# Performance work log

Hardware: AMD Instinct MI355X
Metric: run time of the kernel (lower is better)

## Reference

```python
import jax, jax.numpy as jnp
import numpy as np

N_NODES = 100000
N_EDGES = 1600000
D_FEAT = 64
D_OUT = 64


def setup_inputs() -> dict:
    key = jax.random.key(0)
    k1, k2, k3, k4 = jax.random.split(key, 4)
    vertices = jax.random.normal(k1, (N_NODES, D_FEAT), dtype=jnp.float32)
    edges = jax.random.randint(k2, (2, N_EDGES), 0, N_NODES, dtype=jnp.int64)
    weight = jax.random.normal(k3, (D_OUT, D_FEAT), dtype=jnp.float32) * (1.0 / np.sqrt(D_FEAT))
    bias = jax.random.normal(k4, (D_OUT,), dtype=jnp.float32) * 0.01
    return {"vertices": vertices, "edges": edges, "weight": weight, "bias": bias}


def reference(vertices, edges, weight, bias):
    # GraphConv forward, dense (non-sparse) path, self_loop=True, normalize=True.
    n_vertices = vertices.shape[0]
    idx = jnp.arange(n_vertices, dtype=edges.dtype)
    dst = jnp.concatenate([edges[0], idx])  # scatter destinations (edges[0])
    src = jnp.concatenate([edges[1], idx])  # gather sources (edges[1])
    # agg[i] = sum over edges with dst==i of vertices[src]
    agg = jax.ops.segment_sum(vertices[src], dst, num_segments=n_vertices)
    # degree per node (torch scatters ones_like(neighbours): all feature cols equal)
    deg = jax.ops.segment_sum(
        jnp.ones_like(dst, dtype=vertices.dtype), dst, num_segments=n_vertices
    )
    agg = agg * (jnp.clip(deg, 1.0, None) ** -0.5)[:, None]
    # Linear: y = agg @ W.T + b
    return agg @ weight.T + bias
```

## Files before the change

### kernel.cpp

```cpp
#include <hip/hip_runtime.h>
#include <hip/hip_fp16.h>

constexpr int N_NODES = 100000;
constexpr int N_EDGES = 1600000;
constexpr int D = 64;

constexpr int SH2    = 7;
constexpr int BSZ    = 1 << SH2;
constexpr int NB     = (N_NODES + BSZ - 1) / BSZ;
constexpr int SPLITB = 256;
constexpr int TILE   = (N_EDGES + SPLITB - 1) / SPLITB;
constexpr int LINB   = 2048;

constexpr int SCAN_CHUNK = 1024;
constexpr int NCHUNK = (N_NODES + SCAN_CHUNK - 1) / SCAN_CHUNK;

__global__ __launch_bounds__(256) void lin_hist(
    const float* __restrict__ vertices,
    const float* __restrict__ weight,
    __half* __restrict__ Yh,
    const int* __restrict__ edges,
    int* __restrict__ H)
{
    if (blockIdx.x < LINB) {
        __shared__ float rowbuf[4][64];
        const int wid  = threadIdx.x >> 6;
        const int lane = threadIdx.x & 63;

        float w[64];
        #pragma unroll
        for (int f = 0; f < 64; ++f) w[f] = weight[lane * 64 + f];

        const int nodesPerIter = LINB * 4;
        for (int base = blockIdx.x * 4; base < N_NODES; base += nodesPerIter) {
            const int node = base + wid;
            float a = 0.0f;
            if (node < N_NODES) a = vertices[(size_t)node * D + lane];
            rowbuf[wid][lane] = a;
            __syncthreads();
            float acc = 0.0f;
            #pragma unroll
            for (int f = 0; f < 64; ++f)
                acc += rowbuf[wid][f] * w[f];
            if (node < N_NODES) Yh[(size_t)node * D + lane] = __float2half(acc);
            __syncthreads();
        }
    } else {
        __shared__ int h[NB];
        const int b = blockIdx.x - LINB;
        for (int i = threadIdx.x; i < NB; i += 256) h[i] = 0;
        __syncthreads();
        const int lo = b * TILE;
        const int hi = min(lo + TILE, N_EDGES);
        for (int e = lo + threadIdx.x; e < hi; e += 256)
            atomicAdd(&h[edges[e] >> SH2], 1);
        __syncthreads();
        for (int i = threadIdx.x; i < NB; i += 256)
            H[b * NB + i] = h[i];
    }
}

__global__ __launch_bounds__(256) void s_scanA(int* __restrict__ H,
                                               int* __restrict__ colsum)
{
    const int j = blockIdx.x;
    const int t = threadIdx.x;
    int v = H[t * NB + j];
    __shared__ int s[256];
    s[t] = v; __syncthreads();
    for (int o = 1; o < 256; o <<= 1) {
        int u = (t >= o) ? s[t - o] : 0;
        __syncthreads();
        s[t] += u;
        __syncthreads();
    }
    H[t * NB + j] = s[t] - v;
    if (t == 255) colsum[j] = s[t];
}

__global__ void s_scanB(const int* __restrict__ colsum, int* __restrict__ bbase)
{
    __shared__ int s[256];
    const int t = threadIdx.x;
    int v[4]; int loc = 0;
    #pragma unroll
    for (int k = 0; k < 4; ++k) {
        int i = t * 4 + k;
        v[k] = (i < NB) ? colsum[i] : 0;
        loc += v[k];
    }
    s[t] = loc; __syncthreads();
    for (int o = 1; o < 256; o <<= 1) {
        int u = (t >= o) ? s[t - o] : 0;
        __syncthreads();
        s[t] += u;
        __syncthreads();
    }
    int excl = s[t] - loc;
    #pragma unroll
    for (int k = 0; k < 4; ++k) {
        int i = t * 4 + k;
        if (i < NB) bbase[i] = excl;
        excl += v[k];
    }
}

__global__ __launch_bounds__(256) void s_scatter(const int* __restrict__ edges,
                                                 const int* __restrict__ H,
                                                 const int* __restrict__ bbase,
                                                 int* __restrict__ packed)
{
    __shared__ int cur[NB];
    for (int i = threadIdx.x; i < NB; i += 256)
        cur[i] = bbase[i] + H[blockIdx.x * NB + i];
    __syncthreads();
    const int lo = blockIdx.x * TILE;
    const int hi = min(lo + TILE, N_EDGES);
    for (int e = lo + threadIdx.x; e < hi; e += 256) {
        int dst = edges[e];
        int src = edges[N_EDGES + e];
        int pos = atomicAdd(&cur[dst >> SH2], 1);
        packed[pos] = (src << SH2) | (dst & (BSZ - 1));
    }
}

__global__ __launch_bounds__(256) void bucket_csr(const int* __restrict__ packed,
                                                  const int* __restrict__ bbase,
                                                  const int* __restrict__ colsum,
                                                  int* __restrict__ offsets,
                                                  int* __restrict__ deg,
                                                  int* __restrict__ srt)
{
    __shared__ int h2[BSZ];
    __shared__ int cur2[BSZ];
    __shared__ int s[BSZ];
    const int b = blockIdx.x;
    const int t = threadIdx.x;
    const int start = bbase[b];
    const int cnt   = colsum[b];

    if (t < BSZ) h2[t] = 0;
    __syncthreads();
    for (int i = t; i < cnt; i += 256)
        atomicAdd(&h2[packed[start + i] & (BSZ - 1)], 1);
    __syncthreads();

    if (t < BSZ) s[t] = h2[t];
    __syncthreads();
    for (int o = 1; o < BSZ; o <<= 1) {
        int u = (t >= o && t < BSZ) ? s[t - o] : 0;
        __syncthreads();
        if (t < BSZ) s[t] += u;
        __syncthreads();
    }
    if (t < BSZ) {
        int excl = s[t] - h2[t];
        int node = (b << SH2) + t;
        if (node < N_NODES) { offsets[node] = start + excl; deg[node] = h2[t]; }
        cur2[t] = excl;
    }
    __syncthreads();

    for (int i = t; i < cnt; i += 256) {
        int p = packed[start + i];
        int r = atomicAdd(&cur2[p & (BSZ - 1)], 1);
        srt[start + r] = p >> SH2;
    }
}

__device__ __forceinline__ void addrow(float* acc, uint4 u)
{
    const __half2* h = reinterpret_cast<const __half2*>(&u);
    #pragma unroll
    for (int k = 0; k < 4; ++k) {
        float2 f = __half22float2(h[k]);
        acc[2 * k]     += f.x;
        acc[2 * k + 1] += f.y;
    }
}

__global__ __launch_bounds__(256) void gather_h(
    const __half* __restrict__ Yh,
    const int* __restrict__ offsets,
    const int* __restrict__ deg,
    const int* __restrict__ srt,
    const float* __restrict__ bias,
    float* __restrict__ out)
{
    const int wid  = threadIdx.x >> 6;
    const int lane = threadIdx.x & 63;
    const int g    = lane >> 3;
    const int sub  = lane & 7;
    const int node = blockIdx.x * 4 + wid;
    if (node >= N_NODES) return;

    const int start = offsets[node];
    const int cnt   = deg[node];

    float acc[8];
    #pragma unroll
    for (int j = 0; j < 8; ++j) acc[j] = 0.0f;

    if (g == 0) {
        uint4 u = *reinterpret_cast<const uint4*>(Yh + (size_t)node * D + sub * 8);
        addrow(acc, u);
    }

    int e = 0;
    for (; e + 16 <= cnt; e += 16) {
        int s0 = srt[start + e + g];
        int s1 = srt[start + e + 8 + g];
        uint4 u0 = *reinterpret_cast<const uint4*>(Yh + (size_t)s0 * D + sub * 8);
        uint4 u1 = *reinterpret_cast<const uint4*>(Yh + (size_t)s1 * D + sub * 8);
        addrow(acc, u0);
        addrow(acc, u1);
    }
    if (e + 8 <= cnt) {
        int s0 = srt[start + e + g];
        uint4 u0 = *reinterpret_cast<const uint4*>(Yh + (size_t)s0 * D + sub * 8);
        addrow(acc, u0);
        e += 8;
    }
    if (e + g < cnt) {
        int s0 = srt[start + e + g];
        uint4 u0 = *reinterpret_cast<const uint4*>(Yh + (size_t)s0 * D + sub * 8);
        addrow(acc, u0);
    }

    #pragma unroll
    for (int j = 0; j < 8; ++j) {
        acc[j] += __shfl_xor(acc[j], 8, 64);
        acc[j] += __shfl_xor(acc[j], 16, 64);
        acc[j] += __shfl_xor(acc[j], 32, 64);
    }

    if (g == 0) {
        const float sc = rsqrtf((float)cnt + 1.0f);
        const float4 b0 = *reinterpret_cast<const float4*>(bias + sub * 8);
        const float4 b1 = *reinterpret_cast<const float4*>(bias + sub * 8 + 4);
        float4 r0, r1;
        r0.x = acc[0] * sc + b0.x;  r0.y = acc[1] * sc + b0.y;
        r0.z = acc[2] * sc + b0.z;  r0.w = acc[3] * sc + b0.w;
        r1.x = acc[4] * sc + b1.x;  r1.y = acc[5] * sc + b1.y;
        r1.z = acc[6] * sc + b1.z;  r1.w = acc[7] * sc + b1.w;
        *reinterpret_cast<float4*>(out + (size_t)node * D + sub * 8)     = r0;
        *reinterpret_cast<float4*>(out + (size_t)node * D + sub * 8 + 4) = r1;
    }
}


__global__ __launch_bounds__(256) void linear_kernel(
    const float* __restrict__ vertices,
    const float* __restrict__ weight,
    float* __restrict__ Y)
{
    __shared__ float rowbuf[4][64];
    const int wid  = threadIdx.x >> 6;
    const int lane = threadIdx.x & 63;
    float w[64];
    #pragma unroll
    for (int f = 0; f < 64; ++f) w[f] = weight[lane * 64 + f];
    const int nodesPerIter = gridDim.x * 4;
    for (int base = blockIdx.x * 4; base < N_NODES; base += nodesPerIter) {
        const int node = base + wid;
        float a = 0.0f;
        if (node < N_NODES) a = vertices[(size_t)node * D + lane];
        rowbuf[wid][lane] = a;
        __syncthreads();
        float acc = 0.0f;
        #pragma unroll
        for (int f = 0; f < 64; ++f)
            acc += rowbuf[wid][f] * w[f];
        if (node < N_NODES) Y[(size_t)node * D + lane] = acc;
        __syncthreads();
    }
}

__global__ __launch_bounds__(256) void gather_f32(
    const float* __restrict__ Y,
    const int* __restrict__ offsets,
    const int* __restrict__ deg,
    const int* __restrict__ sortedSrc,
    const float* __restrict__ bias,
    float* __restrict__ out)
{
    const int wid  = threadIdx.x >> 6;
    const int lane = threadIdx.x & 63;
    const int g    = lane >> 4;
    const int sub  = lane & 15;
    const int node = blockIdx.x * 4 + wid;
    if (node >= N_NODES) return;

    const int start = offsets[node];
    const int cnt   = deg[node];

    float4 acc;
    if (g == 0) {
        acc = *reinterpret_cast<const float4*>(Y + (size_t)node * D + (sub << 2));
    } else {
        acc.x = 0.0f; acc.y = 0.0f; acc.z = 0.0f; acc.w = 0.0f;
    }

    int e = 0;
    for (; e + 8 <= cnt; e += 8) {
        int s0 = sortedSrc[start + e + g];
        int s1 = sortedSrc[start + e + 4 + g];
        const float4 a0 = *reinterpret_cast<const float4*>(Y + (size_t)s0 * D + (sub << 2));
        const float4 a1 = *reinterpret_cast<const float4*>(Y + (size_t)s1 * D + (sub << 2));
        acc.x += a0.x; acc.y += a0.y; acc.z += a0.z; acc.w += a0.w;
        acc.x += a1.x; acc.y += a1.y; acc.z += a1.z; acc.w += a1.w;
    }
    if (e + 4 <= cnt) {
        int s0 = sortedSrc[start + e + g];
        const float4 a0 = *reinterpret_cast<const float4*>(Y + (size_t)s0 * D + (sub << 2));
        acc.x += a0.x; acc.y += a0.y; acc.z += a0.z; acc.w += a0.w;
        e += 4;
    }
    if (e + g < cnt) {
        int s0 = sortedSrc[start + e + g];
        const float4 a0 = *reinterpret_cast<const float4*>(Y + (size_t)s0 * D + (sub << 2));
        acc.x += a0.x; acc.y += a0.y; acc.z += a0.z; acc.w += a0.w;
    }

    acc.x += __shfl_xor(acc.x, 16, 64);
    acc.y += __shfl_xor(acc.y, 16, 64);
    acc.z += __shfl_xor(acc.z, 16, 64);
    acc.w += __shfl_xor(acc.w, 16, 64);
    acc.x += __shfl_xor(acc.x, 32, 64);
    acc.y += __shfl_xor(acc.y, 32, 64);
    acc.z += __shfl_xor(acc.z, 32, 64);
    acc.w += __shfl_xor(acc.w, 32, 64);

    if (lane < 16) {
        const float sc = rsqrtf((float)cnt + 1.0f);
        const float4 b4 = *reinterpret_cast<const float4*>(bias + (sub << 2));
        float4 r;
        r.x = acc.x * sc + b4.x;
        r.y = acc.y * sc + b4.y;
        r.z = acc.z * sc + b4.z;
        r.w = acc.w * sc + b4.w;
        *reinterpret_cast<float4*>(out + (size_t)node * D + (sub << 2)) = r;
    }
}

__global__ __launch_bounds__(256) void hist_kernel(const int* __restrict__ edges,
                                                   int* __restrict__ deg)
{
    int e = blockIdx.x * 256 + threadIdx.x;
    if (e < N_EDGES) atomicAdd(&deg[edges[e]], 1);
}

__global__ __launch_bounds__(256) void scan_part(const int* __restrict__ deg,
                                                 int* __restrict__ partial)
{
    int t = threadIdx.x;
    int base = blockIdx.x * SCAN_CHUNK + t * 4;
    int s = 0;
    #pragma unroll
    for (int k = 0; k < 4; ++k) { int i = base + k; if (i < N_NODES) s += deg[i]; }
    int lane = t & 63, wid = t >> 6;
    #pragma unroll
    for (int off = 32; off; off >>= 1) s += __shfl_down(s, off, 64);
    __shared__ int red[4];
    if (lane == 0) red[wid] = s;
    __syncthreads();
    if (t == 0) partial[blockIdx.x] = red[0] + red[1] + red[2] + red[3];
}

__device__ __forceinline__ int waveInclScan(int v, int lane) {
    #pragma unroll
    for (int off = 1; off < 64; off <<= 1) {
        int t = __shfl_up(v, off, 64);
        if (lane >= off) v += t;
    }
    return v;
}

__global__ void scan_small(int* partial) {
    int lane = threadIdx.x;
    int v0 = (lane < NCHUNK) ? partial[lane] : 0;
    int v1 = (64 + lane < NCHUNK) ? partial[64 + lane] : 0;
    int i0 = waveInclScan(v0, lane);
    int tot0 = __shfl(i0, 63, 64);
    int i1 = waveInclScan(v1, lane) + tot0;
    if (lane < NCHUNK) partial[lane] = i0 - v0;
    if (64 + lane < NCHUNK) partial[64 + lane] = i1 - v1;
}

__global__ __launch_bounds__(256) void scan_final(const int* __restrict__ deg,
                                                  const int* __restrict__ partial,
                                                  int* __restrict__ offsets,
                                                  int* __restrict__ cursor)
{
    int t = threadIdx.x;
    int base = blockIdx.x * SCAN_CHUNK + t * 4;
    int d[4]; int s = 0;
    #pragma unroll
    for (int k = 0; k < 4; ++k) { int i = base + k; d[k] = (i < N_NODES) ? deg[i] : 0; s += d[k]; }
    __shared__ int sd[256];
    sd[t] = s; __syncthreads();
    #pragma unroll
    for (int off = 1; off < 256; off <<= 1) {
        int v = (t >= off) ? sd[t - off] : 0;
        __syncthreads();
        sd[t] += v;
        __syncthreads();
    }
    int excl = sd[t] - s + partial[blockIdx.x];
    #pragma unroll
    for (int k = 0; k < 4; ++k) {
        int i = base + k;
        if (i < N_NODES) { offsets[i] = excl; cursor[i] = excl; excl += d[k]; }
    }
}

__global__ __launch_bounds__(256) void scatter_idx(const int* __restrict__ edges,
                                                   int* __restrict__ cursor,
                                                   int* __restrict__ sortedSrc)
{
    int e = blockIdx.x * 256 + threadIdx.x;
    if (e >= N_EDGES) return;
    int dst = edges[e];
    int src = edges[N_EDGES + e];
    int pos = atomicAdd(&cursor[dst], 1);
    sortedSrc[pos] = src;
}


__global__ __launch_bounds__(256) void fb_scatter(
    const float* __restrict__ vertices, const int* __restrict__ edges,
    float* __restrict__ agg, float* __restrict__ degF)
{
    long long tid = (long long)blockIdx.x * 256 + threadIdx.x;
    int lane = threadIdx.x & 63;
    long long e = tid >> 6;
    if (e >= N_EDGES) return;
    int dst = edges[e];
    int src = edges[N_EDGES + e];
    atomicAdd(&agg[(size_t)dst * D + lane], vertices[(size_t)src * D + lane]);
    if (lane == 0) atomicAdd(&degF[dst], 1.0f);
}

__global__ __launch_bounds__(256) void fb_finish(
    const float* __restrict__ vertices, const float* __restrict__ weight,
    const float* __restrict__ bias, const float* __restrict__ degF,
    float* __restrict__ out)
{
    __shared__ float rowbuf[4][64];
    const int wid  = threadIdx.x >> 6;
    const int lane = threadIdx.x & 63;
    float w[64];
    #pragma unroll
    for (int f = 0; f < 64; ++f) w[f] = weight[lane * 64 + f];
    const float b = bias[lane];
    const int nodesPerIter = gridDim.x * 4;
    for (int base = blockIdx.x * 4; base < N_NODES; base += nodesPerIter) {
        const int node = base + wid;
        float a = 0.0f;
        if (node < N_NODES) {
            const float scale = rsqrtf(degF[node] + 1.0f);
            a = (out[(size_t)node * D + lane] + vertices[(size_t)node * D + lane]) * scale;
        }
        rowbuf[wid][lane] = a;
        __syncthreads();
        float acc = b;
        #pragma unroll
        for (int f = 0; f < 64; ++f) acc += rowbuf[wid][f] * w[f];
        if (node < N_NODES) out[(size_t)node * D + lane] = acc;
        __syncthreads();
    }
}

extern "C" void kernel_launch(void* const* d_in, const int* in_sizes, int n_in,
                              void* d_out, int out_size, void* d_ws, size_t ws_size,
                              hipStream_t stream) {
    const float* vertices = (const float*)d_in[0];
    const int*   edges    = (const int*)d_in[1];
    const float* weight   = (const float*)d_in[2];
    const float* bias     = (const float*)d_in[3];
    float* out = (float*)d_out;

    const int threads = 256;
    const int edgeBlocks = (N_EDGES + threads - 1) / threads;

    {
        __half* Yh    = (__half*)d_ws;
        int*   H      = (int*)(Yh + (size_t)N_NODES * D);
        int*   colsum = H + SPLITB * NB;
        int*   bbase  = colsum + NB;
        int*   offs   = bbase + NB;
        int*   deg    = offs + N_NODES;
        int*   packed = deg + N_NODES;
        int*   srt    = packed + N_EDGES;
        size_t needed = (size_t)((char*)(srt + N_EDGES) - (char*)d_ws);
        if (ws_size >= needed) {
            lin_hist<<<LINB + SPLITB, threads, 0, stream>>>(vertices, weight, Yh, edges, H);
            s_scanA<<<NB, threads, 0, stream>>>(H, colsum);
            s_scanB<<<1, threads, 0, stream>>>(colsum, bbase);
            s_scatter<<<SPLITB, threads, 0, stream>>>(edges, H, bbase, packed);
            bucket_csr<<<NB, threads, 0, stream>>>(packed, bbase, colsum, offs, deg, srt);
            gather_h<<<(N_NODES + 3) / 4, threads, 0, stream>>>(Yh, offs, deg, srt, bias, out);
            return;
        }
    }

    {
        float* Y       = (float*)d_ws;
        int*   deg     = (int*)(Y + (size_t)N_NODES * D);
        int*   offs    = deg + N_NODES;
        int*   cursor  = offs + N_NODES;
        int*   partial = cursor + N_NODES;
        int*   srt     = partial + 128;
        size_t needed  = (size_t)((char*)(srt + N_EDGES) - (char*)d_ws);
        if (ws_size >= needed) {
            hipMemsetAsync(deg, 0, sizeof(int) * N_NODES, stream);
            linear_kernel<<<1024, threads, 0, stream>>>(vertices, weight, Y);
            hist_kernel<<<edgeBlocks, threads, 0, stream>>>(edges, deg);
            scan_part<<<NCHUNK, threads, 0, stream>>>(deg, partial);
            scan_small<<<1, 64, 0, stream>>>(partial);
            scan_final<<<NCHUNK, threads, 0, stream>>>(deg, partial, offs, cursor);
            scatter_idx<<<edgeBlocks, threads, 0, stream>>>(edges, cursor, srt);
            gather_f32<<<(N_NODES + 3) / 4, threads, 0, stream>>>(Y, offs, deg, srt, bias, out);
            return;
        }
    }

    {
        float* degF = (float*)d_ws;
        hipMemsetAsync(out, 0, sizeof(float) * (size_t)N_NODES * D, stream);
        hipMemsetAsync(degF, 0, sizeof(float) * N_NODES, stream);
        const long long totalScatter = (long long)N_EDGES * 64;
        fb_scatter<<<(int)((totalScatter + threads - 1) / threads), threads, 0, stream>>>(
            vertices, edges, out, degF);
        fb_finish<<<1024, threads, 0, stream>>>(vertices, weight, bias, degF, out);
    }
}
```

Measured before the change: 116.2 us.

## Fuse bucket CSR build with gather and fold bucket scan into scatter

Shrinks buckets to 64 nodes and fuses the per-bucket counting sort with the neighbor gather, so sorted source indices stay in shared memory (with a global fallback when a bucket exceeds capacity) rather than being written and re-read through offsets/deg/srt arrays. The separate bucket-base scan kernel is removed; every scatter block redundantly scans the column sums itself, and block 0 writes bbase. The linear/histogram kernel moves to 1024-thread blocks with float4 shared reads. This saves two launches and global round-trips, but adds redundant scan work in each scatter block and puts both the per-bucket sort and the gather inside one block with serialized phases.

```diff
diff --git a/kernel.cpp b/kernel.cpp
--- a/kernel.cpp
+++ b/kernel.cpp
@@ -5,17 +5,18 @@
 constexpr int N_EDGES = 1600000;
 constexpr int D = 64;
 
-constexpr int SH2    = 7;
+constexpr int SH2    = 6;
 constexpr int BSZ    = 1 << SH2;
 constexpr int NB     = (N_NODES + BSZ - 1) / BSZ;
 constexpr int SPLITB = 256;
 constexpr int TILE   = (N_EDGES + SPLITB - 1) / SPLITB;
-constexpr int LINB   = 2048;
+constexpr int LINB   = 512;
+constexpr int SRTCAP = 2048;
 
 constexpr int SCAN_CHUNK = 1024;
 constexpr int NCHUNK = (N_NODES + SCAN_CHUNK - 1) / SCAN_CHUNK;
 
-__global__ __launch_bounds__(256) void lin_hist(
+__global__ __launch_bounds__(1024) void lin_hist(
     const float* __restrict__ vertices,
     const float* __restrict__ weight,
     __half* __restrict__ Yh,
@@ -23,7 +24,7 @@
     int* __restrict__ H)
 {
     if (blockIdx.x < LINB) {
-        __shared__ float rowbuf[4][64];
+        __shared__ float rowbuf[16][64];
         const int wid  = threadIdx.x >> 6;
         const int lane = threadIdx.x & 63;
 
@@ -31,31 +32,34 @@
         #pragma unroll
         for (int f = 0; f < 64; ++f) w[f] = weight[lane * 64 + f];
 
-        const int nodesPerIter = LINB * 4;
-        for (int base = blockIdx.x * 4; base < N_NODES; base += nodesPerIter) {
+        const int nodesPerIter = LINB * 16;
+        for (int base = blockIdx.x * 16; base < N_NODES; base += nodesPerIter) {
             const int node = base + wid;
             float a = 0.0f;
             if (node < N_NODES) a = vertices[(size_t)node * D + lane];
             rowbuf[wid][lane] = a;
             __syncthreads();
             float acc = 0.0f;
+            const float4* rb4 = reinterpret_cast<const float4*>(&rowbuf[wid][0]);
             #pragma unroll
-            for (int f = 0; f < 64; ++f)
-                acc += rowbuf[wid][f] * w[f];
+            for (int f4 = 0; f4 < 16; ++f4) {
+                float4 r = rb4[f4];
+                acc += r.x * w[4*f4] + r.y * w[4*f4+1] + r.z * w[4*f4+2] + r.w * w[4*f4+3];
+            }
             if (node < N_NODES) Yh[(size_t)node * D + lane] = __float2half(acc);
             __syncthreads();
         }
     } else {
         __shared__ int h[NB];
         const int b = blockIdx.x - LINB;
-        for (int i = threadIdx.x; i < NB; i += 256) h[i] = 0;
+        for (int i = threadIdx.x; i < NB; i += 1024) h[i] = 0;
         __syncthreads();
         const int lo = b * TILE;
         const int hi = min(lo + TILE, N_EDGES);
-        for (int e = lo + threadIdx.x; e < hi; e += 256)
+        for (int e = lo + threadIdx.x; e < hi; e += 1024)
             atomicAdd(&h[edges[e] >> SH2], 1);
         __syncthreads();
-        for (int i = threadIdx.x; i < NB; i += 256)
+        for (int i = threadIdx.x; i < NB; i += 1024)
             H[b * NB + i] = h[i];
     }
 }
@@ -78,45 +82,40 @@
     if (t == 255) colsum[j] = s[t];
 }
 
-__global__ void s_scanB(const int* __restrict__ colsum, int* __restrict__ bbase)
-{
-    __shared__ int s[256];
+__global__ __launch_bounds__(1024) void s_scatter(const int* __restrict__ edges,
+                                                  const int* __restrict__ H,
+                                                  const int* __restrict__ colsum,
+                                                  int* __restrict__ packed,
+                                                  int* __restrict__ bbase)
+{
+    __shared__ int cur[NB];
+    __shared__ int sd[1024];
     const int t = threadIdx.x;
-    int v[4]; int loc = 0;
-    #pragma unroll
-    for (int k = 0; k < 4; ++k) {
-        int i = t * 4 + k;
-        v[k] = (i < NB) ? colsum[i] : 0;
-        loc += v[k];
-    }
-    s[t] = loc; __syncthreads();
-    for (int o = 1; o < 256; o <<= 1) {
-        int u = (t >= o) ? s[t - o] : 0;
-        __syncthreads();
-        s[t] += u;
-        __syncthreads();
-    }
-    int excl = s[t] - loc;
-    #pragma unroll
-    for (int k = 0; k < 4; ++k) {
-        int i = t * 4 + k;
-        if (i < NB) bbase[i] = excl;
-        excl += v[k];
-    }
-}
-
-__global__ __launch_bounds__(256) void s_scatter(const int* __restrict__ edges,
-                                                 const int* __restrict__ H,
-                                                 const int* __restrict__ bbase,
-                                                 int* __restrict__ packed)
-{
-    __shared__ int cur[NB];
-    for (int i = threadIdx.x; i < NB; i += 256)
-        cur[i] = bbase[i] + H[blockIdx.x * NB + i];
+
+    int v0 = (2*t     < NB) ? colsum[2*t]     : 0;
+    int v1 = (2*t + 1 < NB) ? colsum[2*t + 1] : 0;
+    int pair = v0 + v1;
+    sd[t] = pair; __syncthreads();
+    for (int o = 1; o < 1024; o <<= 1) {
+        int u = (t >= o) ? sd[t - o] : 0;
+        __syncthreads();
+        sd[t] += u;
+        __syncthreads();
+    }
+    int excl = sd[t] - pair;
+    if (2*t < NB) {
+        cur[2*t] = excl + H[blockIdx.x * NB + 2*t];
+        if (blockIdx.x == 0) bbase[2*t] = excl;
+    }
+    if (2*t + 1 < NB) {
+        cur[2*t + 1] = excl + v0 + H[blockIdx.x * NB + 2*t + 1];
+        if (blockIdx.x == 0) bbase[2*t + 1] = excl + v0;
+    }
     __syncthreads();
+
     const int lo = blockIdx.x * TILE;
     const int hi = min(lo + TILE, N_EDGES);
-    for (int e = lo + threadIdx.x; e < hi; e += 256) {
+    for (int e = lo + t; e < hi; e += 1024) {
         int dst = edges[e];
         int src = edges[N_EDGES + e];
         int pos = atomicAdd(&cur[dst >> SH2], 1);
@@ -124,50 +123,6 @@
     }
 }
 
-__global__ __launch_bounds__(256) void bucket_csr(const int* __restrict__ packed,
-                                                  const int* __restrict__ bbase,
-                                                  const int* __restrict__ colsum,
-                                                  int* __restrict__ offsets,
-                                                  int* __restrict__ deg,
-                                                  int* __restrict__ srt)
-{
-    __shared__ int h2[BSZ];
-    __shared__ int cur2[BSZ];
-    __shared__ int s[BSZ];
-    const int b = blockIdx.x;
-    const int t = threadIdx.x;
-    const int start = bbase[b];
-    const int cnt   = colsum[b];
-
-    if (t < BSZ) h2[t] = 0;
-    __syncthreads();
-    for (int i = t; i < cnt; i += 256)
-        atomicAdd(&h2[packed[start + i] & (BSZ - 1)], 1);
-    __syncthreads();
-
-    if (t < BSZ) s[t] = h2[t];
-    __syncthreads();
-    for (int o = 1; o < BSZ; o <<= 1) {
-        int u = (t >= o && t < BSZ) ? s[t - o] : 0;
-        __syncthreads();
-        if (t < BSZ) s[t] += u;
-        __syncthreads();
-    }
-    if (t < BSZ) {
-        int excl = s[t] - h2[t];
-        int node = (b << SH2) + t;
-        if (node < N_NODES) { offsets[node] = start + excl; deg[node] = h2[t]; }
-        cur2[t] = excl;
-    }
-    __syncthreads();
-
-    for (int i = t; i < cnt; i += 256) {
-        int p = packed[start + i];
-        int r = atomicAdd(&cur2[p & (BSZ - 1)], 1);
-        srt[start + r] = p >> SH2;
-    }
-}
-
 __device__ __forceinline__ void addrow(float* acc, uint4 u)
 {
     const __half2* h = reinterpret_cast<const __half2*>(&u);
@@ -179,72 +134,148 @@
     }
 }
 
-__global__ __launch_bounds__(256) void gather_h(
+__device__ __forceinline__ int waveInclScan(int v, int lane) {
+    #pragma unroll
+    for (int off = 1; off < 64; off <<= 1) {
+        int t = __shfl_up(v, off, 64);
+        if (lane >= off) v += t;
+    }
+    return v;
+}
+
+__global__ __launch_bounds__(256) void csr_gather(
+    const int* __restrict__ packed,
+    const int* __restrict__ bbase,
+    const int* __restrict__ colsum,
     const __half* __restrict__ Yh,
-    const int* __restrict__ offsets,
-    const int* __restrict__ deg,
-    const int* __restrict__ srt,
     const float* __restrict__ bias,
+    int* __restrict__ srtG,
     float* __restrict__ out)
 {
-    const int wid  = threadIdx.x >> 6;
-    const int lane = threadIdx.x & 63;
+    __shared__ int h[BSZ];
+    __shared__ int excl[BSZ];
+    __shared__ int cur[BSZ];
+    __shared__ int srtL[SRTCAP];
+
+    const int t = threadIdx.x;
+    const int b = blockIdx.x;
+    const int start = bbase[b];
+    const int cnt   = colsum[b];
+
+    if (t < BSZ) h[t] = 0;
+    __syncthreads();
+    for (int i = t; i < cnt; i += 256)
+        atomicAdd(&h[packed[start + i] & (BSZ - 1)], 1);
+    __syncthreads();
+    if (t < BSZ) {
+        int v = h[t];
+        int incl = waveInclScan(v, t);
+        excl[t] = incl - v;
+        cur[t]  = incl - v;
+    }
+    __syncthreads();
+    const bool useG = (cnt > SRTCAP);
+    if (!useG) {
+        for (int i = t; i < cnt; i += 256) {
+            int p = packed[start + i];
+            int r = atomicAdd(&cur[p & (BSZ - 1)], 1);
+            srtL[r] = p >> SH2;
+        }
+    } else {
+        for (int i = t; i < cnt; i += 256) {
+            int p = packed[start + i];
+            int r = atomicAdd(&cur[p & (BSZ - 1)], 1);
+            srtG[start + r] = p >> SH2;
+        }
+    }
+    __syncthreads();
+
+    const int wid  = t >> 6;
+    const int lane = t & 63;
     const int g    = lane >> 3;
     const int sub  = lane & 7;
-    const int node = blockIdx.x * 4 + wid;
-    if (node >= N_NODES) return;
-
-    const int start = offsets[node];
-    const int cnt   = deg[node];
-
-    float acc[8];
-    #pragma unroll
-    for (int j = 0; j < 8; ++j) acc[j] = 0.0f;
-
-    if (g == 0) {
-        uint4 u = *reinterpret_cast<const uint4*>(Yh + (size_t)node * D + sub * 8);
-        addrow(acc, u);
-    }
-
-    int e = 0;
-    for (; e + 16 <= cnt; e += 16) {
-        int s0 = srt[start + e + g];
-        int s1 = srt[start + e + 8 + g];
-        uint4 u0 = *reinterpret_cast<const uint4*>(Yh + (size_t)s0 * D + sub * 8);
-        uint4 u1 = *reinterpret_cast<const uint4*>(Yh + (size_t)s1 * D + sub * 8);
-        addrow(acc, u0);
-        addrow(acc, u1);
-    }
-    if (e + 8 <= cnt) {
-        int s0 = srt[start + e + g];
-        uint4 u0 = *reinterpret_cast<const uint4*>(Yh + (size_t)s0 * D + sub * 8);
-        addrow(acc, u0);
-        e += 8;
-    }
-    if (e + g < cnt) {
-        int s0 = srt[start + e + g];
-        uint4 u0 = *reinterpret_cast<const uint4*>(Yh + (size_t)s0 * D + sub * 8);
-        addrow(acc, u0);
-    }
-
-    #pragma unroll
-    for (int j = 0; j < 8; ++j) {
-        acc[j] += __shfl_xor(acc[j], 8, 64);
-        acc[j] += __shfl_xor(acc[j], 16, 64);
-        acc[j] += __shfl_xor(acc[j], 32, 64);
-    }
-
-    if (g == 0) {
-        const float sc = rsqrtf((float)cnt + 1.0f);
-        const float4 b0 = *reinterpret_cast<const float4*>(bias + sub * 8);
-        const float4 b1 = *reinterpret_cast<const float4*>(bias + sub * 8 + 4);
-        float4 r0, r1;
-        r0.x = acc[0] * sc + b0.x;  r0.y = acc[1] * sc + b0.y;
-        r0.z = acc[2] * sc + b0.z;  r0.w = acc[3] * sc + b0.w;
-        r1.x = acc[4] * sc + b1.x;  r1.y = acc[5] * sc + b1.y;
-        r1.z = acc[6] * sc + b1.z;  r1.w = acc[7] * sc + b1.w;
-        *reinterpret_cast<float4*>(out + (size_t)node * D + sub * 8)     = r0;
-        *reinterpret_cast<float4*>(out + (size_t)node * D + sub * 8 + 4) = r1;
+
+    const float4 b0 = *reinterpret_cast<const float4*>(bias + sub * 8);
+    const float4 b1 = *reinterpret_cast<const float4*>(bias + sub * 8 + 4);
+
+    for (int m = 0; m < 16; ++m) {
+        const int l = wid * 16 + m;
+        const int node = (b << SH2) + l;
+        if (node >= N_NODES) break;
+
+        const int off = excl[l];
+        const int dc  = h[l];
+
+        float acc[8];
+        #pragma unroll
+        for (int j = 0; j < 8; ++j) acc[j] = 0.0f;
+
+        if (g == 0) {
+            uint4 u = *reinterpret_cast<const uint4*>(Yh + (size_t)node * D + sub * 8);
+            addrow(acc, u);
+        }
+
+        int e = 0;
+        if (!useG) {
+            for (; e + 16 <= dc; e += 16) {
+                int s0 = srtL[off + e + g];
+                int s1 = srtL[off + e + 8 + g];
+                uint4 u0 = *reinterpret_cast<const uint4*>(Yh + (size_t)s0 * D + sub * 8);
+                uint4 u1 = *reinterpret_cast<const uint4*>(Yh + (size_t)s1 * D + sub * 8);
+                addrow(acc, u0);
+                addrow(acc, u1);
+            }
+            if (e + 8 <= dc) {
+                int s0 = srtL[off + e + g];
+                uint4 u0 = *reinterpret_cast<const uint4*>(Yh + (size_t)s0 * D + sub * 8);
+                addrow(acc, u0);
+                e += 8;
+            }
+            if (e + g < dc) {
+                int s0 = srtL[off + e + g];
+                uint4 u0 = *reinterpret_cast<const uint4*>(Yh + (size_t)s0 * D + sub * 8);
+                addrow(acc, u0);
+            }
+        } else {
+            const int* srt = srtG + start;
+            for (; e + 16 <= dc; e += 16) {
+                int s0 = srt[off + e + g];
+                int s1 = srt[off + e + 8 + g];
+                uint4 u0 = *reinterpret_cast<const uint4*>(Yh + (size_t)s0 * D + sub * 8);
+                uint4 u1 = *reinterpret_cast<const uint4*>(Yh + (size_t)s1 * D + sub * 8);
+                addrow(acc, u0);
+                addrow(acc, u1);
+            }
+            if (e + 8 <= dc) {
+                int s0 = srt[off + e + g];
+                uint4 u0 = *reinterpret_cast<const uint4*>(Yh + (size_t)s0 * D + sub * 8);
+                addrow(acc, u0);
+                e += 8;
+            }
+            if (e + g < dc) {
+                int s0 = srt[off + e + g];
+                uint4 u0 = *reinterpret_cast<const uint4*>(Yh + (size_t)s0 * D + sub * 8);
+                addrow(acc, u0);
+            }
+        }
+
+        #pragma unroll
+        for (int j = 0; j < 8; ++j) {
+            acc[j] += __shfl_xor(acc[j], 8, 64);
+            acc[j] += __shfl_xor(acc[j], 16, 64);
+            acc[j] += __shfl_xor(acc[j], 32, 64);
+        }
+
+        if (g == 0) {
+            const float sc = rsqrtf((float)dc + 1.0f);
+            float4 r0, r1;
+            r0.x = acc[0] * sc + b0.x;  r0.y = acc[1] * sc + b0.y;
+            r0.z = acc[2] * sc + b0.z;  r0.w = acc[3] * sc + b0.w;
+            r1.x = acc[4] * sc + b1.x;  r1.y = acc[5] * sc + b1.y;
+            r1.z = acc[6] * sc + b1.z;  r1.w = acc[7] * sc + b1.w;
+            *reinterpret_cast<float4*>(out + (size_t)node * D + sub * 8)     = r0;
+            *reinterpret_cast<float4*>(out + (size_t)node * D + sub * 8 + 4) = r1;
+        }
     }
 }
 
@@ -367,15 +398,6 @@
     if (t == 0) partial[blockIdx.x] = red[0] + red[1] + red[2] + red[3];
 }
 
-__device__ __forceinline__ int waveInclScan(int v, int lane) {
-    #pragma unroll
-    for (int off = 1; off < 64; off <<= 1) {
-        int t = __shfl_up(v, off, 64);
-        if (lane >= off) v += t;
-    }
-    return v;
-}
-
 __global__ void scan_small(int* partial) {
     int lane = threadIdx.x;
     int v0 = (lane < NCHUNK) ? partial[lane] : 0;
@@ -488,18 +510,14 @@
         int*   H      = (int*)(Yh + (size_t)N_NODES * D);
         int*   colsum = H + SPLITB * NB;
         int*   bbase  = colsum + NB;
-        int*   offs   = bbase + NB;
-        int*   deg    = offs + N_NODES;
-        int*   packed = deg + N_NODES;
-        int*   srt    = packed + N_EDGES;
-        size_t needed = (size_t)((char*)(srt + N_EDGES) - (char*)d_ws);
+        int*   packed = bbase + NB;
+        int*   srtG   = packed + N_EDGES;
+        size_t needed = (size_t)((char*)(srtG + N_EDGES) - (char*)d_ws);
         if (ws_size >= needed) {
-            lin_hist<<<LINB + SPLITB, threads, 0, stream>>>(vertices, weight, Yh, edges, H);
+            lin_hist<<<LINB + SPLITB, 1024, 0, stream>>>(vertices, weight, Yh, edges, H);
             s_scanA<<<NB, threads, 0, stream>>>(H, colsum);
-            s_scanB<<<1, threads, 0, stream>>>(colsum, bbase);
-            s_scatter<<<SPLITB, threads, 0, stream>>>(edges, H, bbase, packed);
-            bucket_csr<<<NB, threads, 0, stream>>>(packed, bbase, colsum, offs, deg, srt);
-            gather_h<<<(N_NODES + 3) / 4, threads, 0, stream>>>(Yh, offs, deg, srt, bias, out);
+            s_scatter<<<SPLITB, 1024, 0, stream>>>(edges, H, colsum, packed, bbase);
+            csr_gather<<<NB, threads, 0, stream>>>(packed, bbase, colsum, Yh, bias, srtG, out);
             return;
         }
     }
```

After: 141.3 us. 21.6% more time.

## Replace per-block histogram scan with global atomic bucket counts and tile cursors

Applied to the files above, without the earlier changes.

The two-level counting sort no longer stores a per-block histogram matrix and scans it column-wise. Blocks now add their local bucket counts into a global count array with atomics, a single 512-thread kernel scans the counts, and the scatter kernel reserves a range per tile through atomics on a global cursor. Bucket size drops from 128 to 64 nodes, so the in-bucket scan becomes a wave shuffle scan. This removes two kernels and the large histogram traffic, at the cost of a memset, more global atomics, and a nondeterministic edge order within each bucket.

```diff
diff --git a/kernel.cpp b/kernel.cpp
--- a/kernel.cpp
+++ b/kernel.cpp
@@ -5,22 +5,33 @@
 constexpr int N_EDGES = 1600000;
 constexpr int D = 64;
 
-constexpr int SH2    = 7;
+constexpr int SH2    = 6;
 constexpr int BSZ    = 1 << SH2;
 constexpr int NB     = (N_NODES + BSZ - 1) / BSZ;
 constexpr int SPLITB = 256;
 constexpr int TILE   = (N_EDGES + SPLITB - 1) / SPLITB;
 constexpr int LINB   = 2048;
+constexpr int TILE3  = 4096;
+constexpr int NBLK3  = (N_EDGES + TILE3 - 1) / TILE3;
 
 constexpr int SCAN_CHUNK = 1024;
 constexpr int NCHUNK = (N_NODES + SCAN_CHUNK - 1) / SCAN_CHUNK;
+
+__device__ __forceinline__ int waveInclScan(int v, int lane) {
+    #pragma unroll
+    for (int off = 1; off < 64; off <<= 1) {
+        int t = __shfl_up(v, off, 64);
+        if (lane >= off) v += t;
+    }
+    return v;
+}
 
 __global__ __launch_bounds__(256) void lin_hist(
     const float* __restrict__ vertices,
     const float* __restrict__ weight,
     __half* __restrict__ Yh,
     const int* __restrict__ edges,
-    int* __restrict__ H)
+    int* __restrict__ bcnt)
 {
     if (blockIdx.x < LINB) {
         __shared__ float rowbuf[4][64];
@@ -55,42 +66,28 @@
         for (int e = lo + threadIdx.x; e < hi; e += 256)
             atomicAdd(&h[edges[e] >> SH2], 1);
         __syncthreads();
-        for (int i = threadIdx.x; i < NB; i += 256)
-            H[b * NB + i] = h[i];
-    }
-}
-
-__global__ __launch_bounds__(256) void s_scanA(int* __restrict__ H,
-                                               int* __restrict__ colsum)
-{
-    const int j = blockIdx.x;
-    const int t = threadIdx.x;
-    int v = H[t * NB + j];
-    __shared__ int s[256];
-    s[t] = v; __syncthreads();
-    for (int o = 1; o < 256; o <<= 1) {
-        int u = (t >= o) ? s[t - o] : 0;
-        __syncthreads();
-        s[t] += u;
-        __syncthreads();
-    }
-    H[t * NB + j] = s[t] - v;
-    if (t == 255) colsum[j] = s[t];
-}
-
-__global__ void s_scanB(const int* __restrict__ colsum, int* __restrict__ bbase)
-{
-    __shared__ int s[256];
+        for (int i = threadIdx.x; i < NB; i += 256) {
+            int v = h[i];
+            if (v) atomicAdd(&bcnt[i], v);
+        }
+    }
+}
+
+__global__ __launch_bounds__(512) void scan_init(const int* __restrict__ bcnt,
+                                                 int* __restrict__ bbase,
+                                                 int* __restrict__ cursor)
+{
+    __shared__ int s[512];
     const int t = threadIdx.x;
     int v[4]; int loc = 0;
     #pragma unroll
     for (int k = 0; k < 4; ++k) {
         int i = t * 4 + k;
-        v[k] = (i < NB) ? colsum[i] : 0;
+        v[k] = (i < NB) ? bcnt[i] : 0;
         loc += v[k];
     }
     s[t] = loc; __syncthreads();
-    for (int o = 1; o < 256; o <<= 1) {
+    for (int o = 1; o < 512; o <<= 1) {
         int u = (t >= o) ? s[t - o] : 0;
         __syncthreads();
         s[t] += u;
@@ -100,67 +97,79 @@
     #pragma unroll
     for (int k = 0; k < 4; ++k) {
         int i = t * 4 + k;
-        if (i < NB) bbase[i] = excl;
+        if (i < NB) { bbase[i] = excl; cursor[i] = excl; }
         excl += v[k];
     }
 }
 
-__global__ __launch_bounds__(256) void s_scatter(const int* __restrict__ edges,
-                                                 const int* __restrict__ H,
-                                                 const int* __restrict__ bbase,
+__global__ __launch_bounds__(512) void s_scatter(const int* __restrict__ edges,
+                                                 int* __restrict__ cursor,
                                                  int* __restrict__ packed)
 {
-    __shared__ int cur[NB];
-    for (int i = threadIdx.x; i < NB; i += 256)
-        cur[i] = bbase[i] + H[blockIdx.x * NB + i];
-    __syncthreads();
-    const int lo = blockIdx.x * TILE;
-    const int hi = min(lo + TILE, N_EDGES);
-    for (int e = lo + threadIdx.x; e < hi; e += 256) {
-        int dst = edges[e];
-        int src = edges[N_EDGES + e];
-        int pos = atomicAdd(&cur[dst >> SH2], 1);
-        packed[pos] = (src << SH2) | (dst & (BSZ - 1));
+    __shared__ int h[NB];
+    __shared__ int base[NB];
+    const int t = threadIdx.x;
+    const int lo = blockIdx.x * TILE3;
+
+    for (int i = t; i < NB; i += 512) h[i] = 0;
+    __syncthreads();
+
+    int myd[8];
+    #pragma unroll
+    for (int k = 0; k < 8; ++k) {
+        int e = lo + k * 512 + t;
+        myd[k] = (e < N_EDGES) ? edges[e] : -1;
+        if (myd[k] >= 0) atomicAdd(&h[myd[k] >> SH2], 1);
+    }
+    __syncthreads();
+
+    for (int j = t; j < NB; j += 512) {
+        int c = h[j];
+        base[j] = c ? atomicAdd(&cursor[j], c) : 0;
+        h[j] = 0;
+    }
+    __syncthreads();
+
+    #pragma unroll
+    for (int k = 0; k < 8; ++k) {
+        if (myd[k] >= 0) {
+            int e = lo + k * 512 + t;
+            int src = edges[N_EDGES + e];
+            int j = myd[k] >> SH2;
+            int r = atomicAdd(&h[j], 1);
+            packed[base[j] + r] = (src << SH2) | (myd[k] & (BSZ - 1));
+        }
     }
 }
 
 __global__ __launch_bounds__(256) void bucket_csr(const int* __restrict__ packed,
                                                   const int* __restrict__ bbase,
-                                                  const int* __restrict__ colsum,
+                                                  const int* __restrict__ bcnt,
                                                   int* __restrict__ offsets,
                                                   int* __restrict__ deg,
                                                   int* __restrict__ srt)
 {
     __shared__ int h2[BSZ];
     __shared__ int cur2[BSZ];
-    __shared__ int s[BSZ];
     const int b = blockIdx.x;
     const int t = threadIdx.x;
     const int start = bbase[b];
-    const int cnt   = colsum[b];
+    const int cnt   = bcnt[b];
 
     if (t < BSZ) h2[t] = 0;
     __syncthreads();
     for (int i = t; i < cnt; i += 256)
         atomicAdd(&h2[packed[start + i] & (BSZ - 1)], 1);
     __syncthreads();
-
-    if (t < BSZ) s[t] = h2[t];
-    __syncthreads();
-    for (int o = 1; o < BSZ; o <<= 1) {
-        int u = (t >= o && t < BSZ) ? s[t - o] : 0;
-        __syncthreads();
-        if (t < BSZ) s[t] += u;
-        __syncthreads();
-    }
     if (t < BSZ) {
-        int excl = s[t] - h2[t];
+        int v = h2[t];
+        int incl = waveInclScan(v, t);
+        int excl = incl - v;
         int node = (b << SH2) + t;
-        if (node < N_NODES) { offsets[node] = start + excl; deg[node] = h2[t]; }
+        if (node < N_NODES) { offsets[node] = start + excl; deg[node] = v; }
         cur2[t] = excl;
     }
     __syncthreads();
-
     for (int i = t; i < cnt; i += 256) {
         int p = packed[start + i];
         int r = atomicAdd(&cur2[p & (BSZ - 1)], 1);
@@ -367,15 +376,6 @@
     if (t == 0) partial[blockIdx.x] = red[0] + red[1] + red[2] + red[3];
 }
 
-__device__ __forceinline__ int waveInclScan(int v, int lane) {
-    #pragma unroll
-    for (int off = 1; off < 64; off <<= 1) {
-        int t = __shfl_up(v, off, 64);
-        if (lane >= off) v += t;
-    }
-    return v;
-}
-
 __global__ void scan_small(int* partial) {
     int lane = threadIdx.x;
     int v0 = (lane < NCHUNK) ? partial[lane] : 0;
@@ -485,20 +485,20 @@
 
     {
         __half* Yh    = (__half*)d_ws;
-        int*   H      = (int*)(Yh + (size_t)N_NODES * D);
-        int*   colsum = H + SPLITB * NB;
-        int*   bbase  = colsum + NB;
-        int*   offs   = bbase + NB;
+        int*   bcnt   = (int*)(Yh + (size_t)N_NODES * D);
+        int*   bbase  = bcnt + NB;
+        int*   cursor = bbase + NB;
+        int*   offs   = cursor + NB;
         int*   deg    = offs + N_NODES;
         int*   packed = deg + N_NODES;
         int*   srt    = packed + N_EDGES;
         size_t needed = (size_t)((char*)(srt + N_EDGES) - (char*)d_ws);
         if (ws_size >= needed) {
-            lin_hist<<<LINB + SPLITB, threads, 0, stream>>>(vertices, weight, Yh, edges, H);
-            s_scanA<<<NB, threads, 0, stream>>>(H, colsum);
-            s_scanB<<<1, threads, 0, stream>>>(colsum, bbase);
-            s_scatter<<<SPLITB, threads, 0, stream>>>(edges, H, bbase, packed);
-            bucket_csr<<<NB, threads, 0, stream>>>(packed, bbase, colsum, offs, deg, srt);
+            hipMemsetAsync(bcnt, 0, sizeof(int) * NB, stream);
+            lin_hist<<<LINB + SPLITB, threads, 0, stream>>>(vertices, weight, Yh, edges, bcnt);
+            scan_init<<<1, 512, 0, stream>>>(bcnt, bbase, cursor);
+            s_scatter<<<NBLK3, 512, 0, stream>>>(edges, cursor, packed);
+            bucket_csr<<<NB, threads, 0, stream>>>(packed, bbase, bcnt, offs, deg, srt);
             gather_h<<<(N_NODES + 3) / 4, threads, 0, stream>>>(Yh, offs, deg, srt, bias, out);
             return;
         }
```

New measurement: 136.9 us. +17.8%, slower.

## Coarsen CSR buckets to 512 nodes and fuse scans into atomic-cursor scatter

Applied to the files above, without the earlier changes.

Replaces the 128-node bucket, 256-way per-block histogram plus two scan kernels with 196 coarse buckets of 512 nodes. Global bucket counts are accumulated with atomics, and each scatter block recomputes the small prefix scan itself, then claims contiguous output chunks per bucket through a global atomic cursor. This removes two kernel launches and the large H matrix traffic. In exchange it adds a memset, makes the packed order within a bucket nondeterministic, and uses 1024-thread blocks for the second-level CSR pass over larger buckets, which lowers parallelism.

```diff
diff --git a/kernel.cpp b/kernel.cpp
--- a/kernel.cpp
+++ b/kernel.cpp
@@ -5,22 +5,33 @@
 constexpr int N_EDGES = 1600000;
 constexpr int D = 64;
 
-constexpr int SH2    = 7;
-constexpr int BSZ    = 1 << SH2;
-constexpr int NB     = (N_NODES + BSZ - 1) / BSZ;
+constexpr int SHC    = 9;
+constexpr int BSZC   = 1 << SHC;
+constexpr int NBC    = (N_NODES + BSZC - 1) / BSZC;
 constexpr int SPLITB = 256;
 constexpr int TILE   = (N_EDGES + SPLITB - 1) / SPLITB;
 constexpr int LINB   = 2048;
+constexpr int TILE2  = 8192;
+constexpr int NBLK2  = (N_EDGES + TILE2 - 1) / TILE2;
 
 constexpr int SCAN_CHUNK = 1024;
 constexpr int NCHUNK = (N_NODES + SCAN_CHUNK - 1) / SCAN_CHUNK;
+
+__device__ __forceinline__ int waveInclScan(int v, int lane) {
+    #pragma unroll
+    for (int off = 1; off < 64; off <<= 1) {
+        int t = __shfl_up(v, off, 64);
+        if (lane >= off) v += t;
+    }
+    return v;
+}
 
 __global__ __launch_bounds__(256) void lin_hist(
     const float* __restrict__ vertices,
     const float* __restrict__ weight,
     __half* __restrict__ Yh,
     const int* __restrict__ edges,
-    int* __restrict__ H)
+    int* __restrict__ bcntC)
 {
     if (blockIdx.x < LINB) {
         __shared__ float rowbuf[4][64];
@@ -46,125 +57,120 @@
             __syncthreads();
         }
     } else {
-        __shared__ int h[NB];
+        __shared__ int h[NBC];
         const int b = blockIdx.x - LINB;
-        for (int i = threadIdx.x; i < NB; i += 256) h[i] = 0;
+        if (threadIdx.x < NBC) h[threadIdx.x] = 0;
         __syncthreads();
         const int lo = b * TILE;
         const int hi = min(lo + TILE, N_EDGES);
         for (int e = lo + threadIdx.x; e < hi; e += 256)
-            atomicAdd(&h[edges[e] >> SH2], 1);
-        __syncthreads();
-        for (int i = threadIdx.x; i < NB; i += 256)
-            H[b * NB + i] = h[i];
-    }
-}
-
-__global__ __launch_bounds__(256) void s_scanA(int* __restrict__ H,
-                                               int* __restrict__ colsum)
-{
-    const int j = blockIdx.x;
+            atomicAdd(&h[edges[e] >> SHC], 1);
+        __syncthreads();
+        if (threadIdx.x < NBC) {
+            int v = h[threadIdx.x];
+            if (v) atomicAdd(&bcntC[threadIdx.x], v);
+        }
+    }
+}
+
+__global__ __launch_bounds__(1024) void s_scatter(const int* __restrict__ edges,
+                                                  const int* __restrict__ bcntC,
+                                                  int* __restrict__ cursorDelta,
+                                                  int* __restrict__ bbaseC,
+                                                  int* __restrict__ packed)
+{
+    __shared__ int s[256];
+    __shared__ int baseC[NBC];
+    __shared__ int h[NBC];
+    __shared__ int chunk[NBC];
     const int t = threadIdx.x;
-    int v = H[t * NB + j];
-    __shared__ int s[256];
-    s[t] = v; __syncthreads();
+
+    int v = 0;
+    if (t < 256) { v = (t < NBC) ? bcntC[t] : 0; s[t] = v; }
+    __syncthreads();
     for (int o = 1; o < 256; o <<= 1) {
-        int u = (t >= o) ? s[t - o] : 0;
-        __syncthreads();
-        s[t] += u;
-        __syncthreads();
-    }
-    H[t * NB + j] = s[t] - v;
-    if (t == 255) colsum[j] = s[t];
-}
-
-__global__ void s_scanB(const int* __restrict__ colsum, int* __restrict__ bbase)
-{
-    __shared__ int s[256];
-    const int t = threadIdx.x;
-    int v[4]; int loc = 0;
-    #pragma unroll
-    for (int k = 0; k < 4; ++k) {
-        int i = t * 4 + k;
-        v[k] = (i < NB) ? colsum[i] : 0;
-        loc += v[k];
-    }
-    s[t] = loc; __syncthreads();
-    for (int o = 1; o < 256; o <<= 1) {
-        int u = (t >= o) ? s[t - o] : 0;
-        __syncthreads();
-        s[t] += u;
-        __syncthreads();
-    }
-    int excl = s[t] - loc;
-    #pragma unroll
-    for (int k = 0; k < 4; ++k) {
-        int i = t * 4 + k;
-        if (i < NB) bbase[i] = excl;
-        excl += v[k];
-    }
-}
-
-__global__ __launch_bounds__(256) void s_scatter(const int* __restrict__ edges,
-                                                 const int* __restrict__ H,
-                                                 const int* __restrict__ bbase,
-                                                 int* __restrict__ packed)
-{
-    __shared__ int cur[NB];
-    for (int i = threadIdx.x; i < NB; i += 256)
-        cur[i] = bbase[i] + H[blockIdx.x * NB + i];
-    __syncthreads();
-    const int lo = blockIdx.x * TILE;
-    const int hi = min(lo + TILE, N_EDGES);
-    for (int e = lo + threadIdx.x; e < hi; e += 256) {
-        int dst = edges[e];
-        int src = edges[N_EDGES + e];
-        int pos = atomicAdd(&cur[dst >> SH2], 1);
-        packed[pos] = (src << SH2) | (dst & (BSZ - 1));
-    }
-}
-
-__global__ __launch_bounds__(256) void bucket_csr(const int* __restrict__ packed,
-                                                  const int* __restrict__ bbase,
-                                                  const int* __restrict__ colsum,
-                                                  int* __restrict__ offsets,
-                                                  int* __restrict__ deg,
-                                                  int* __restrict__ srt)
-{
-    __shared__ int h2[BSZ];
-    __shared__ int cur2[BSZ];
-    __shared__ int s[BSZ];
+        int u = (t < 256 && t >= o) ? s[t - o] : 0;
+        __syncthreads();
+        if (t < 256) s[t] += u;
+        __syncthreads();
+    }
+    if (t < NBC) {
+        int e = s[t] - v;
+        baseC[t] = e;
+        h[t] = 0;
+        if (blockIdx.x == 0) bbaseC[t] = e;
+    }
+    __syncthreads();
+
+    const int lo = blockIdx.x * TILE2;
+    int myd[8];
+    #pragma unroll
+    for (int k = 0; k < 8; ++k) {
+        int e = lo + k * 1024 + t;
+        myd[k] = (e < N_EDGES) ? edges[e] : -1;
+        if (myd[k] >= 0) atomicAdd(&h[myd[k] >> SHC], 1);
+    }
+    __syncthreads();
+
+    if (t < NBC) {
+        int c = h[t];
+        chunk[t] = c ? (baseC[t] + atomicAdd(&cursorDelta[t], c)) : 0;
+        h[t] = 0;
+    }
+    __syncthreads();
+
+    #pragma unroll
+    for (int k = 0; k < 8; ++k) {
+        if (myd[k] >= 0) {
+            int e = lo + k * 1024 + t;
+            int src = edges[N_EDGES + e];
+            int j = myd[k] >> SHC;
+            int r = atomicAdd(&h[j], 1);
+            packed[chunk[j] + r] = (src << SHC) | (myd[k] & (BSZC - 1));
+        }
+    }
+}
+
+__global__ __launch_bounds__(1024) void csr512(const int* __restrict__ packed,
+                                               const int* __restrict__ bbaseC,
+                                               const int* __restrict__ bcntC,
+                                               int* __restrict__ offsets,
+                                               int* __restrict__ deg,
+                                               int* __restrict__ srt)
+{
+    __shared__ int h2[BSZC];
+    __shared__ int cur2[BSZC];
+    __shared__ int s[BSZC];
     const int b = blockIdx.x;
     const int t = threadIdx.x;
-    const int start = bbase[b];
-    const int cnt   = colsum[b];
-
-    if (t < BSZ) h2[t] = 0;
-    __syncthreads();
-    for (int i = t; i < cnt; i += 256)
-        atomicAdd(&h2[packed[start + i] & (BSZ - 1)], 1);
-    __syncthreads();
-
-    if (t < BSZ) s[t] = h2[t];
-    __syncthreads();
-    for (int o = 1; o < BSZ; o <<= 1) {
-        int u = (t >= o && t < BSZ) ? s[t - o] : 0;
-        __syncthreads();
-        if (t < BSZ) s[t] += u;
-        __syncthreads();
-    }
-    if (t < BSZ) {
+    const int start = bbaseC[b];
+    const int cnt   = bcntC[b];
+
+    if (t < BSZC) h2[t] = 0;
+    __syncthreads();
+    for (int i = t; i < cnt; i += 1024)
+        atomicAdd(&h2[packed[start + i] & (BSZC - 1)], 1);
+    __syncthreads();
+
+    if (t < BSZC) s[t] = h2[t];
+    __syncthreads();
+    for (int o = 1; o < BSZC; o <<= 1) {
+        int u = (t < BSZC && t >= o) ? s[t - o] : 0;
+        __syncthreads();
+        if (t < BSZC) s[t] += u;
+        __syncthreads();
+    }
+    if (t < BSZC) {
         int excl = s[t] - h2[t];
-        int node = (b << SH2) + t;
+        int node = (b << SHC) + t;
         if (node < N_NODES) { offsets[node] = start + excl; deg[node] = h2[t]; }
         cur2[t] = excl;
     }
     __syncthreads();
-
-    for (int i = t; i < cnt; i += 256) {
+    for (int i = t; i < cnt; i += 1024) {
         int p = packed[start + i];
-        int r = atomicAdd(&cur2[p & (BSZ - 1)], 1);
-        srt[start + r] = p >> SH2;
+        int r = atomicAdd(&cur2[p & (BSZC - 1)], 1);
+        srt[start + r] = p >> SHC;
     }
 }
 
@@ -367,15 +373,6 @@
     if (t == 0) partial[blockIdx.x] = red[0] + red[1] + red[2] + red[3];
 }
 
-__device__ __forceinline__ int waveInclScan(int v, int lane) {
-    #pragma unroll
-    for (int off = 1; off < 64; off <<= 1) {
-        int t = __shfl_up(v, off, 64);
-        if (lane >= off) v += t;
-    }
-    return v;
-}
-
 __global__ void scan_small(int* partial) {
     int lane = threadIdx.x;
     int v0 = (lane < NCHUNK) ? partial[lane] : 0;
@@ -484,21 +481,20 @@
     const int edgeBlocks = (N_EDGES + threads - 1) / threads;
 
     {
-        __half* Yh    = (__half*)d_ws;
-        int*   H      = (int*)(Yh + (size_t)N_NODES * D);
-        int*   colsum = H + SPLITB * NB;
-        int*   bbase  = colsum + NB;
-        int*   offs   = bbase + NB;
-        int*   deg    = offs + N_NODES;
-        int*   packed = deg + N_NODES;
-        int*   srt    = packed + N_EDGES;
-        size_t needed = (size_t)((char*)(srt + N_EDGES) - (char*)d_ws);
+        __half* Yh         = (__half*)d_ws;
+        int*   bcntC       = (int*)(Yh + (size_t)N_NODES * D);
+        int*   cursorDelta = bcntC + NBC;
+        int*   bbaseC      = cursorDelta + NBC;
+        int*   offs        = bbaseC + NBC;
+        int*   deg         = offs + N_NODES;
+        int*   packed      = deg + N_NODES;
+        int*   srt         = packed + N_EDGES;
+        size_t needed      = (size_t)((char*)(srt + N_EDGES) - (char*)d_ws);
         if (ws_size >= needed) {
-            lin_hist<<<LINB + SPLITB, threads, 0, stream>>>(vertices, weight, Yh, edges, H);
-            s_scanA<<<NB, threads, 0, stream>>>(H, colsum);
-            s_scanB<<<1, threads, 0, stream>>>(colsum, bbase);
-            s_scatter<<<SPLITB, threads, 0, stream>>>(edges, H, bbase, packed);
-            bucket_csr<<<NB, threads, 0, stream>>>(packed, bbase, colsum, offs, deg, srt);
+            hipMemsetAsync(bcntC, 0, sizeof(int) * 2 * NBC, stream);
+            lin_hist<<<LINB + SPLITB, threads, 0, stream>>>(vertices, weight, Yh, edges, bcntC);
+            s_scatter<<<NBLK2, 1024, 0, stream>>>(edges, bcntC, cursorDelta, bbaseC, packed);
+            csr512<<<NBC, 1024, 0, stream>>>(packed, bbaseC, bcntC, offs, deg, srt);
             gather_h<<<(N_NODES + 3) / 4, threads, 0, stream>>>(Yh, offs, deg, srt, bias, out);
             return;
         }
```

Result: slower. 118.8 us (+2.2%).
